# Kernel tuning notes

Measured on AMD Instinct MI355X. Metric: run time of the kernel, lower is better.

The kernel has to match this reference:

```python
import jax, jax.numpy as jnp
import numpy as np
import math

EPS = 1e-6


def setup_inputs() -> dict:
    key = jax.random.key(0)
    k1, k2, k3 = jax.random.split(key, 3)
    B, S, D = 8, 2048, 256
    return {
        "query": jax.random.normal(k1, (B, S, D), dtype=jnp.float32),
        "keys": jax.random.normal(k2, (B, S, D), dtype=jnp.float32),
        "values": jax.random.normal(k3, (B, S, D), dtype=jnp.float32),
        "c": jnp.asarray(0.01, dtype=jnp.float32),  # learned curvature parameter
    }


def reference(query, keys, values, c):
    # query/keys: [B,S,D], values: [B,S,Dv]
    scale = math.sqrt(query.shape[-1])
    q2 = jnp.sum(query * query, axis=-1)            # [B,S]  |q_i|^2
    k2 = jnp.sum(keys * keys, axis=-1)              # [B,S]  |k_j|^2
    cross = jnp.einsum("bid,bjd->bij", query, keys)  # [B,S,S]
    # squared pairwise distance via identity, avoiding the [B,S,S,D] diff tensor
    nd2 = jnp.maximum(q2[:, :, None] + k2[:, None, :] - 2.0 * cross, 0.0)
    # faithful to original: denom pairs query row i with key row i (broadcast quirk)
    denom = jnp.maximum((1.0 - c * q2) * (1.0 - c * k2), EPS)  # [B,S]
    arg = jnp.maximum(1.0 + 2.0 * c * nd2 / denom[:, :, None], 1.0 + EPS)
    dist = jnp.arccosh(arg)                          # [B,S,S]
    attn = jax.nn.softmax(-dist / scale, axis=-1)
    return jnp.einsum("bij,bjd->bid", attn, values)
```

## Files before the change

kernel.cpp:

```cpp
#include <hip/hip_runtime.h>

#define B_N   8
#define S_LEN 2048
#define D_DIM 256

typedef __attribute__((ext_vector_type(4)))  float          f32x4;
typedef __attribute__((ext_vector_type(16))) float          f32x16;
typedef __attribute__((ext_vector_type(8)))  short          s16x8;
typedef __attribute__((ext_vector_type(8)))  __bf16         b16x8;
typedef __attribute__((ext_vector_type(8)))  unsigned short u16x8;
typedef __attribute__((ext_vector_type(4)))  unsigned int   u32x4;

__device__ __forceinline__ unsigned short f2bf(float f) {
    unsigned u = __builtin_bit_cast(unsigned, f);
    u += 0x7FFFu + ((u >> 16) & 1u);
    return (unsigned short)(u >> 16);
}
__device__ __forceinline__ u16x8 pack8(f32x4 a, f32x4 b) {
    u16x8 o;
#pragma unroll
    for (int u = 0; u < 4; ++u) { o[u] = f2bf(a[u]); o[u + 4] = f2bf(b[u]); }
    return o;
}
__device__ __forceinline__ f32x16 zero16() {
    f32x16 z;
#pragma unroll
    for (int i = 0; i < 16; ++i) z[i] = 0.f;
    return z;
}
__device__ __forceinline__ unsigned cvtpk(float lo, float hi) {
    unsigned r;
    asm("v_cvt_pk_bf16_f32 %0, %1, %2" : "=v"(r) : "v"(lo), "v"(hi));
    return r;
}
__device__ __forceinline__ void xswap(unsigned& x, unsigned& y, int lh) {
    unsigned vs = lh ? x : y;
    unsigned vr = (unsigned)__shfl_xor((int)vs, 32, 64);
    x = lh ? vr : x;
    y = lh ? y : vr;
}
__device__ __forceinline__ float hw_sqrt(float x) {
    float r; asm("v_sqrt_f32 %0, %1" : "=v"(r) : "v"(x)); return r;
}
__device__ __forceinline__ float hw_log2(float x) {
    float r; asm("v_log_f32 %0, %1" : "=v"(r) : "v"(x)); return r;
}
__device__ __forceinline__ float hw_exp2(float x) {
    float r; asm("v_exp_f32 %0, %1" : "=v"(r) : "v"(x)); return r;
}
__device__ __forceinline__ float hw_rcp(float x) {
    float r; asm("v_rcp_f32 %0, %1" : "=v"(r) : "v"(x)); return r;
}
__device__ __forceinline__ void gload16(const void* g, void* l) {
    __builtin_amdgcn_global_load_lds((const __attribute__((address_space(1))) void*)g,
                                     (__attribute__((address_space(3))) void*)l, 16, 0, 0);
}

template <typename A>
__device__ __forceinline__ auto mfma3216_(A a, A b, f32x16 c, int)
    -> decltype(__builtin_amdgcn_mfma_f32_32x32x16_bf16(a, b, c, 0, 0, 0)) {
    return __builtin_amdgcn_mfma_f32_32x32x16_bf16(a, b, c, 0, 0, 0);
}
template <typename A>
__device__ __forceinline__ f32x16 mfma3216_(A a, A b, f32x16 c, long) {
    b16x8 a2 = __builtin_bit_cast(b16x8, a);
    b16x8 b2 = __builtin_bit_cast(b16x8, b);
    return __builtin_amdgcn_mfma_f32_32x32x16_bf16(a2, b2, c, 0, 0, 0);
}
__device__ __forceinline__ f32x16 MFMA(u16x8 a, u16x8 b, f32x16 c) {
    return mfma3216_(__builtin_bit_cast(s16x8, a), __builtin_bit_cast(s16x8, b), c, 0);
}

__global__ void __launch_bounds__(256) prep_rows(const float* __restrict__ Q,
                                                 const float* __restrict__ K,
                                                 const float* __restrict__ cp,
                                                 float* __restrict__ q2g,
                                                 float* __restrict__ k2g,
                                                 float* __restrict__ cfg) {
    const int w = threadIdx.x >> 6, l = threadIdx.x & 63;
    const float c = *cp;
#pragma unroll 1
    for (int p = 0; p < 16; ++p) {
        const int row = blockIdx.x * 64 + p * 4 + w;
        f32x4 qv = *((const f32x4*)(Q + (size_t)row * D_DIM) + l);
        f32x4 kv = *((const f32x4*)(K + (size_t)row * D_DIM) + l);
        float sq = qv[0]*qv[0] + qv[1]*qv[1] + qv[2]*qv[2] + qv[3]*qv[3];
        float sk = kv[0]*kv[0] + kv[1]*kv[1] + kv[2]*kv[2] + kv[3]*kv[3];
#pragma unroll
        for (int m = 1; m < 64; m <<= 1) {
            sq += __shfl_xor(sq, m, 64);
            sk += __shfl_xor(sk, m, 64);
        }
        if (l == 0) {
            q2g[row] = sq;
            k2g[row] = sk;
            float dn = fmaxf((1.f - c * sq) * (1.f - c * sk), 1e-6f);
            cfg[row] = 2.f * c / dn;
        }
    }
}

__global__ void __launch_bounds__(256) cvt_bf16(const float* __restrict__ src,
                                                unsigned short* __restrict__ dst) {
    const size_t i = ((size_t)blockIdx.x * 256 + threadIdx.x) * 8;
    f32x4 a = *(const f32x4*)(src + i);
    f32x4 b = *(const f32x4*)(src + i + 4);
    *(u16x8*)(dst + i) = pack8(a, b);
}

__global__ void __launch_bounds__(256) transp_v(const float* __restrict__ V,
                                                unsigned short* __restrict__ VT) {
    __shared__ float tile[64][65];
    const int bid = blockIdx.x;
    const int b = bid >> 7, rem = bid & 127, jt = rem >> 2, dt = rem & 3;
    const int j0 = jt * 64, d0 = dt * 64;
    const int t = threadIdx.x;
#pragma unroll
    for (int p = 0; p < 4; ++p) {
        const int jr = p * 16 + (t >> 4);
        f32x4 v = *(const f32x4*)(V + (size_t)(b * S_LEN + j0 + jr) * D_DIM + d0 + (t & 15) * 4);
#pragma unroll
        for (int u = 0; u < 4; ++u) tile[jr][(t & 15) * 4 + u] = v[u];
    }
    __syncthreads();
#pragma unroll
    for (int p = 0; p < 2; ++p) {
        const int dr = p * 32 + (t >> 3), seg = t & 7;
        u16x8 o;
#pragma unroll
        for (int u = 0; u < 8; ++u) o[u] = f2bf(tile[seg * 8 + u][dr]);
        *(u16x8*)(VT + (size_t)(b * D_DIM + d0 + dr) * S_LEN + j0 + seg * 8) = o;
    }
}

template <int PRE>
__global__ void __launch_bounds__(256, 2) hyp_attn(
    const float* __restrict__ Qf, const float* __restrict__ Kf, const float* __restrict__ Vf,
    const unsigned short* __restrict__ Kb, const unsigned short* __restrict__ VTg,
    const float* __restrict__ q2g, const float* __restrict__ k2g, const float* __restrict__ cfg,
    float* __restrict__ out) {
    __shared__ __align__(1024) unsigned char tiles[65536];
    __shared__ float k2sh[S_LEN];
    __shared__ float lsumBuf[2][2][32];
    const int bid = blockIdx.x;
    const int nb = (bid & 7) * 64 + (bid >> 3);
    const int b = nb >> 6, rt = nb & 63;
    const int tid = threadIdx.x;
    const int w = tid >> 6, l = tid & 63;
    const int l31 = l & 31, lh = l >> 5;
    const int jsub = w & 1, dh = w >> 1;
    const int qr0 = rt * 32;
    const int qrow = b * S_LEN + qr0 + l31;

    *(f32x4*)&k2sh[tid * 8]     = *(const f32x4*)(k2g + b * S_LEN + tid * 8);
    *(f32x4*)&k2sh[tid * 8 + 4] = *(const f32x4*)(k2g + b * S_LEN + tid * 8 + 4);

    u16x8 qf[16];
    {
        const float* qp = Qf + (size_t)qrow * D_DIM + lh * 8;
#pragma unroll
        for (int ks = 0; ks < 16; ++ks) {
            f32x4 a = *(const f32x4*)(qp + ks * 16);
            f32x4 c4 = *(const f32x4*)(qp + ks * 16 + 4);
            qf[ks] = pack8(a, c4);
        }
    }
    const float q2r = q2g[qrow];
    const float cfr = cfg[qrow];
    const float base1 = fmaf(cfr, q2r, 1.0f);

    f32x16 oacc[4];
#pragma unroll
    for (int i = 0; i < 4; ++i) oacc[i] = zero16();
    float lsum = 0.f;

    const size_t kbBase = (size_t)b * S_LEN * D_DIM;

    auto stageK = [&](int buf, int it) {
        const int j0 = it * 64;
#pragma unroll
        for (int p = 0; p < 8; ++p) {
            const int idx = p * 256 + tid;
            const int row = idx >> 5, sl = idx & 31;
            const unsigned short* gp = Kb + kbBase + (size_t)(j0 + row) * D_DIM
                                     + ((sl ^ (row & 7)) << 3);
            gload16(gp, (char*)tiles + buf * 32768 + idx * 16);
        }
    };
    auto stageK0 = [&](int buf, int it) {
        const int j0 = it * 64;
#pragma unroll
        for (int p = 0; p < 8; ++p) {
            const int idx = p * 256 + tid;
            const int row = idx >> 5, sl = idx & 31;
            const float* sp = Kf + kbBase + (size_t)(j0 + row) * D_DIM
                            + ((sl ^ (row & 7)) << 3);
            *(u16x8*)((char*)tiles + buf * 32768 + idx * 16) =
                pack8(*(const f32x4*)sp, *(const f32x4*)(sp + 4));
        }
    };
    const unsigned short* vbase = VTg + ((size_t)(b * D_DIM + dh * 128 + l31) * S_LEN)
                                + jsub * 32 + lh * 8;
    auto loadVg = [&](int it, u16x8 (&Vr)[8]) {
        const unsigned short* p0 = vbase + it * 64;
#pragma unroll
        for (int db = 0; db < 4; ++db) {
            Vr[db * 2]     = *(const u16x8*)(p0 + (size_t)(db * 32) * S_LEN);
            Vr[db * 2 + 1] = *(const u16x8*)(p0 + (size_t)(db * 32) * S_LEN + 16);
        }
    };
    auto loadV0 = [&](int it, u16x8 (&Vr)[8]) {
        const int j0 = it * 64 + jsub * 32 + lh * 8;
#pragma unroll
        for (int db = 0; db < 4; ++db) {
            const int d = dh * 128 + db * 32 + l31;
            u16x8 o0, o1;
#pragma unroll
            for (int u = 0; u < 8; ++u) {
                o0[u] = f2bf(Vf[kbBase + (size_t)(j0 + u) * D_DIM + d]);
                o1[u] = f2bf(Vf[kbBase + (size_t)(j0 + 16 + u) * D_DIM + d]);
            }
            Vr[db * 2] = o0; Vr[db * 2 + 1] = o1;
        }
    };

    const int xk = (l31 & 7) << 4;
    const char* KBp = (const char*)tiles + (jsub * 32 + l31) * 512;

    if (PRE) {
        stageK(0, 0);
        asm volatile("s_waitcnt vmcnt(0) lgkmcnt(0)" ::: "memory");
        __builtin_amdgcn_s_barrier();
    }

#pragma unroll 1
    for (int it = 0; it < 32; ++it) {
        const int kb = it & 1;
        u16x8 VA[8];
        if (PRE) {
            loadVg(it, VA);
            if (it < 31) stageK(kb ^ 1, it + 1);
        } else {
            stageK0(kb, it);
            loadV0(it, VA);
            __syncthreads();
        }

        f32x16 sacc = zero16();
#pragma unroll
        for (int ks = 0; ks < 16; ++ks) {
            u16x8 kf = *(const u16x8*)(KBp + kb * 32768 + (((ks * 2 + lh) << 4) ^ xk));
            sacc = MFMA(kf, qf[ks], sacc);
        }

        f32x4 k2q[4];
#pragma unroll
        for (int g = 0; g < 4; ++g)
            k2q[g] = *(const f32x4*)&k2sh[it * 64 + jsub * 32 + g * 8 + lh * 4];
#pragma unroll
        for (int r = 0; r < 16; ++r) {
            const float t = fmaf(-2.f, sacc[r], k2q[r >> 2][r & 3]);
            const float arg = fmaxf(fmaf(cfr, t, base1), 1.f + 1e-6f);
            const float y = arg + hw_sqrt(fmaf(arg, arg, -1.f));
            const float p = hw_exp2(hw_log2(y) * -0.0625f);
            lsum += p;
            sacc[r] = p;
        }
        unsigned A_ = cvtpk(sacc[0], sacc[1]),   C_ = cvtpk(sacc[2], sacc[3]);
        unsigned Bv = cvtpk(sacc[4], sacc[5]),   D_ = cvtpk(sacc[6], sacc[7]);
        unsigned E_ = cvtpk(sacc[8], sacc[9]),   G_ = cvtpk(sacc[10], sacc[11]);
        unsigned F_ = cvtpk(sacc[12], sacc[13]), H_ = cvtpk(sacc[14], sacc[15]);
        xswap(A_, Bv, lh); xswap(C_, D_, lh);
        xswap(E_, F_, lh); xswap(G_, H_, lh);
        const u16x8 pa0 = __builtin_bit_cast(u16x8, (u32x4){A_, C_, Bv, D_});
        const u16x8 pa1 = __builtin_bit_cast(u16x8, (u32x4){E_, G_, F_, H_});

#pragma unroll
        for (int db = 0; db < 4; ++db) {
            oacc[db] = MFMA(pa0, VA[db * 2], oacc[db]);
            oacc[db] = MFMA(pa1, VA[db * 2 + 1], oacc[db]);
        }

        if (PRE) {
            asm volatile("s_waitcnt vmcnt(0)" ::: "memory");
            __builtin_amdgcn_s_barrier();
        } else {
            __syncthreads();
        }
    }

    lsum += __shfl_xor(lsum, 32, 64);
    if (lh == 0) lsumBuf[jsub][dh][l31] = lsum;
    float* sf = (float*)tiles;
    if (jsub == 1) {
#pragma unroll
        for (int db = 0; db < 4; ++db)
#pragma unroll
            for (int r = 0; r < 16; ++r) {
                const int crow = (r & 3) + 8 * (r >> 2) + 4 * lh;
                sf[dh * 4096 + crow * 128 + db * 32 + l31] = oacc[db][r];
            }
    }
    __syncthreads();
    if (jsub == 0) {
        float rdn[16];
#pragma unroll
        for (int r = 0; r < 16; ++r) {
            const int crow = (r & 3) + 8 * (r >> 2) + 4 * lh;
            rdn[r] = hw_rcp(lsumBuf[0][dh][crow] + lsumBuf[1][dh][crow]);
        }
#pragma unroll
        for (int db = 0; db < 4; ++db)
#pragma unroll
            for (int r = 0; r < 16; ++r) {
                const int crow = (r & 3) + 8 * (r >> 2) + 4 * lh;
                const float o = oacc[db][r] + sf[dh * 4096 + crow * 128 + db * 32 + l31];
                out[(size_t)(b * S_LEN + qr0 + crow) * D_DIM + dh * 128 + db * 32 + l31]
                    = o * rdn[r];
            }
    }
}

extern "C" void kernel_launch(void* const* d_in, const int* in_sizes, int n_in,
                              void* d_out, int out_size, void* d_ws, size_t ws_size,
                              hipStream_t stream) {
    const float* Q = (const float*)d_in[0];
    const float* K = (const float*)d_in[1];
    const float* V = (const float*)d_in[2];
    const float* cp = (const float*)d_in[3];
    float* out = (float*)d_out;
    (void)in_sizes; (void)n_in; (void)out_size;

    const size_t BS = (size_t)B_N * S_LEN;
    float* q2g = (float*)d_ws;
    float* k2g = q2g + BS;
    float* cfg = k2g + BS;
    unsigned short* Kb = (unsigned short*)(cfg + BS);
    unsigned short* VTg = Kb + BS * D_DIM;
    const size_t need_full = 3 * BS * 4 + 2 * BS * D_DIM * 2;

    prep_rows<<<(B_N * S_LEN) / 64, 256, 0, stream>>>(Q, K, cp, q2g, k2g, cfg);

    if (ws_size >= need_full) {
        cvt_bf16<<<(int)((BS * D_DIM / 8) / 256), 256, 0, stream>>>(K, Kb);
        transp_v<<<B_N * (S_LEN / 64) * (D_DIM / 64), 256, 0, stream>>>(V, VTg);
        hyp_attn<1><<<512, 256, 0, stream>>>(Q, K, V, Kb, VTg, q2g, k2g, cfg, out);
    } else {
        hyp_attn<0><<<512, 256, 0, stream>>>(Q, K, V, Kb, VTg, q2g, k2g, cfg, out);
    }
}
```

Measured before the change: 125.4 us.

## Software-pipeline QK^T of next tile behind softmax and PV of current tile

```diff
diff --git a/kernel.cpp b/kernel.cpp
--- a/kernel.cpp
+++ b/kernel.cpp
@@ -227,64 +227,76 @@
     const int xk = (l31 & 7) << 4;
     const char* KBp = (const char*)tiles + (jsub * 32 + l31) * 512;
 
+    auto qktF = [&](int buf) {
+        f32x16 s = zero16();
+#pragma unroll
+        for (int ks = 0; ks < 16; ++ks) {
+            u16x8 kf = *(const u16x8*)(KBp + buf * 32768 + (((ks * 2 + lh) << 4) ^ xk));
+            s = MFMA(kf, qf[ks], s);
+        }
+        return s;
+    };
+    auto softmaxF = [&](int it, f32x16& s, u16x8& pa0, u16x8& pa1) {
+        f32x4 k2q[4];
+#pragma unroll
+        for (int g = 0; g < 4; ++g)
+            k2q[g] = *(const f32x4*)&k2sh[it * 64 + jsub * 32 + g * 8 + lh * 4];
+#pragma unroll
+        for (int r = 0; r < 16; ++r) {
+            const float t = fmaf(-2.f, s[r], k2q[r >> 2][r & 3]);
+            const float arg = fmaxf(fmaf(cfr, t, base1), 1.f + 1e-6f);
+            const float y = arg + hw_sqrt(fmaf(arg, arg, -1.f));
+            const float p = hw_exp2(hw_log2(y) * -0.0625f);
+            lsum += p;
+            s[r] = p;
+        }
+        unsigned A_ = cvtpk(s[0], s[1]),   C_ = cvtpk(s[2], s[3]);
+        unsigned Bv = cvtpk(s[4], s[5]),   D_ = cvtpk(s[6], s[7]);
+        unsigned E_ = cvtpk(s[8], s[9]),   G_ = cvtpk(s[10], s[11]);
+        unsigned F_ = cvtpk(s[12], s[13]), H_ = cvtpk(s[14], s[15]);
+        xswap(A_, Bv, lh); xswap(C_, D_, lh);
+        xswap(E_, F_, lh); xswap(G_, H_, lh);
+        pa0 = __builtin_bit_cast(u16x8, (u32x4){A_, C_, Bv, D_});
+        pa1 = __builtin_bit_cast(u16x8, (u32x4){E_, G_, F_, H_});
+    };
+    auto pvF = [&](u16x8 pa0, u16x8 pa1, u16x8 (&VA)[8]) {
+#pragma unroll
+        for (int db = 0; db < 4; ++db) {
+            oacc[db] = MFMA(pa0, VA[db * 2], oacc[db]);
+            oacc[db] = MFMA(pa1, VA[db * 2 + 1], oacc[db]);
+        }
+    };
+
     if (PRE) {
         stageK(0, 0);
         asm volatile("s_waitcnt vmcnt(0) lgkmcnt(0)" ::: "memory");
         __builtin_amdgcn_s_barrier();
-    }
-
+        f32x16 sacc = qktF(0);
 #pragma unroll 1
-    for (int it = 0; it < 32; ++it) {
-        const int kb = it & 1;
-        u16x8 VA[8];
-        if (PRE) {
+        for (int it = 0; it < 32; ++it) {
+            u16x8 VA[8];
             loadVg(it, VA);
-            if (it < 31) stageK(kb ^ 1, it + 1);
-        } else {
-            stageK0(kb, it);
+            if (it < 31) stageK((it + 1) & 1, it + 1);
+            u16x8 pa0, pa1;
+            softmaxF(it, sacc, pa0, pa1);
+            asm volatile("s_waitcnt vmcnt(0)" ::: "memory");
+            __builtin_amdgcn_s_barrier();
+            __builtin_amdgcn_s_setprio(1);
+            pvF(pa0, pa1, VA);
+            if (it < 31) sacc = qktF((it + 1) & 1);
+            __builtin_amdgcn_s_setprio(0);
+        }
+    } else {
+#pragma unroll 1
+        for (int it = 0; it < 32; ++it) {
+            u16x8 VA[8];
+            stageK0(0, it);
             loadV0(it, VA);
             __syncthreads();
-        }
-
-        f32x16 sacc = zero16();
-#pragma unroll
-        for (int ks = 0; ks < 16; ++ks) {
-            u16x8 kf = *(const u16x8*)(KBp + kb * 32768 + (((ks * 2 + lh) << 4) ^ xk));
-            sacc = MFMA(kf, qf[ks], sacc);
-        }
-
-        f32x4 k2q[4];
-#pragma unroll
-        for (int g = 0; g < 4; ++g)
-            k2q[g] = *(const f32x4*)&k2sh[it * 64 + jsub * 32 + g * 8 + lh * 4];
-#pragma unroll
-        for (int r = 0; r < 16; ++r) {
-            const float t = fmaf(-2.f, sacc[r], k2q[r >> 2][r & 3]);
-            const float arg = fmaxf(fmaf(cfr, t, base1), 1.f + 1e-6f);
-            const float y = arg + hw_sqrt(fmaf(arg, arg, -1.f));
-            const float p = hw_exp2(hw_log2(y) * -0.0625f);
-            lsum += p;
-            sacc[r] = p;
-        }
-        unsigned A_ = cvtpk(sacc[0], sacc[1]),   C_ = cvtpk(sacc[2], sacc[3]);
-        unsigned Bv = cvtpk(sacc[4], sacc[5]),   D_ = cvtpk(sacc[6], sacc[7]);
-        unsigned E_ = cvtpk(sacc[8], sacc[9]),   G_ = cvtpk(sacc[10], sacc[11]);
-        unsigned F_ = cvtpk(sacc[12], sacc[13]), H_ = cvtpk(sacc[14], sacc[15]);
-        xswap(A_, Bv, lh); xswap(C_, D_, lh);
-        xswap(E_, F_, lh); xswap(G_, H_, lh);
-        const u16x8 pa0 = __builtin_bit_cast(u16x8, (u32x4){A_, C_, Bv, D_});
-        const u16x8 pa1 = __builtin_bit_cast(u16x8, (u32x4){E_, G_, F_, H_});
-
-#pragma unroll
-        for (int db = 0; db < 4; ++db) {
-            oacc[db] = MFMA(pa0, VA[db * 2], oacc[db]);
-            oacc[db] = MFMA(pa1, VA[db * 2 + 1], oacc[db]);
-        }
-
-        if (PRE) {
-            asm volatile("s_waitcnt vmcnt(0)" ::: "memory");
-            __builtin_amdgcn_s_barrier();
-        } else {
+            f32x16 sacc = qktF(0);
+            u16x8 pa0, pa1;
+            softmaxF(it, sacc, pa0, pa1);
+            pvF(pa0, pa1, VA);
             __syncthreads();
         }
     }
```

After: 122.4 us. 1.02x faster.
